# Optimization experiments

Hardware: AMD Instinct MI355X
Metric: run time of the kernel (lower is better)

The kernel has to match this reference:

```python
import jax, jax.numpy as jnp
import numpy as np

B, F, H, W, C = 1, 16, 32, 32, 128


def setup_inputs() -> dict:
    key = jax.random.key(0)
    ks = jax.random.split(key, 6)
    w = lambda k: jax.random.normal(k, (C, C), jnp.float32) * 0.02
    return {
        "x": jax.random.normal(ks[0], (B, F, H, W, C), jnp.float32),
        "gamma": jnp.ones((C,), jnp.float32),
        "wq": w(ks[1]), "bq": jnp.zeros((C,), jnp.float32),
        "wk": w(ks[2]), "bk": jnp.zeros((C,), jnp.float32),
        "wv": w(ks[3]), "bv": jnp.zeros((C,), jnp.float32),
        "wo": w(ks[4]), "bo": jnp.zeros((C,), jnp.float32),
    }


def reference(x, gamma, wq, bq, wk, bk, wv, bv, wo, bo):
    b, f, h, w_, c = x.shape
    s, n_hw = f * h * w_, h * w_
    identity = x

    # RMSNorm variant: L2-normalize over channels, rescale by sqrt(C) * gamma
    xn = x / (jnp.linalg.norm(x, axis=-1, keepdims=True) + 1e-8)
    xn = xn * (c ** 0.5) * gamma

    # 1x1x1 convs == pointwise linear projections; flatten to tokens [b, s, c]
    xn = xn.reshape(b, s, c)
    q = xn @ wq + bq
    k = xn @ wk + bk
    v = xn @ wv + bv

    # frame-causal block mask: query at frame i attends to all keys in frames <= i
    frame = jnp.arange(s) // n_hw                      # [s]
    allowed = frame[:, None] >= frame[None, :]          # [s, s] bool

    scale = 1.0 / jnp.sqrt(c)
    scores = jnp.einsum('bqc,bkc->bqk', q, k) * scale   # [b, s, s]
    scores = jnp.where(allowed, scores, -jnp.inf)
    attn = jax.nn.softmax(scores, axis=-1)
    out = jnp.einsum('bqk,bkc->bqc', attn, v)           # [b, s, c]

    out = out @ wo + bo
    return out.reshape(b, f, h, w_, c) + identity
```

## Files before the change

### kernel.cpp

```cpp
#include <hip/hip_runtime.h>
#include <hip/hip_bf16.h>

typedef __bf16 bf16x8 __attribute__((ext_vector_type(8)));
typedef float f32x4 __attribute__((ext_vector_type(4)));
typedef float f32x16 __attribute__((ext_vector_type(16)));
typedef unsigned short u16;
typedef unsigned int u32;
typedef u16 ushort8 __attribute__((ext_vector_type(8)));
typedef u32 u32x4 __attribute__((ext_vector_type(4)));

#define S_TOK 16384
#define C_DIM 128
#define L2E 1.4426950408889634f
#define QK_SCALE 0.08838834764831845f
#define SQRTC 11.313708498984761f

#define NBLK 512
#define TPB 34

#define WT_OFF   0u
#define BIAS_OFF 131072u
#define XN_OFF   147456u
#define O_OFF    XN_OFF
#define Q_OFF    (XN_OFF + 4194304u)
#define K_OFF    (Q_OFF + 4194304u)
#define VF_OFF   (K_OFF + 4194304u)
#define PART_OFF (VF_OFF + 4194304u)
#define ML_OFF   (PART_OFF + 20971520u)

#define ZERO16 ((f32x16){0.f,0.f,0.f,0.f,0.f,0.f,0.f,0.f,0.f,0.f,0.f,0.f,0.f,0.f,0.f,0.f})

__device__ __forceinline__ int in_is_bf16(const void* gamma) {
  return ((const u16*)gamma)[0] == 0x3F80;
}
__device__ __forceinline__ float ldf(const void* p, int i, int bf) {
  if (bf) { u32 b = ((const u16*)p)[i]; return __uint_as_float(b << 16); }
  return ((const float*)p)[i];
}
__device__ __forceinline__ float b2f(u16 b) { return __uint_as_float((u32)b << 16); }
__device__ __forceinline__ u16 f2b(float f) {
  return __builtin_bit_cast(u16, (__bf16)f);
}
__device__ __forceinline__ void gld16(const void* g, void* l) {
  __builtin_amdgcn_global_load_lds((const __attribute__((address_space(1))) u32*)g,
                                   (__attribute__((address_space(3))) u32*)l, 16, 0, 0);
}
__device__ __forceinline__ int qb_of(int t) {
  int F = 0;
  while (64 * (F + 1) * (F + 2) <= t) F++;
  int span = 16 * (F + 1);
  return 8 * F + (t - 64 * F * (F + 1)) / span;
}
__device__ __forceinline__ int start_of(int qq) {
  int Fq = qq >> 3, iq = qq & 7;
  return 16 * (Fq + 1) * (4 * Fq + iq);
}

__global__ void __launch_bounds__(256) prep_norm_kernel(const void* x, const void* gamma,
    const void* wq, const void* bq, const void* wk, const void* bk,
    const void* wv, const void* bv, const void* wo, const void* bo, char* ws) {
  int bf = in_is_bf16(gamma);
  if (blockIdx.x >= 2048) {
    int bb = blockIdx.x - 2048;
    if (bb < 256) {
      int gid = bb * 256 + threadIdx.x;
      int m = gid >> 14; int rem = gid & 16383;
      int k = rem >> 7; int n = rem & 127;
      const void* W = (m == 0) ? wq : (m == 1) ? wk : (m == 2) ? wv : wo;
      float v = ldf(W, rem, bf);
      if (m == 0) v *= QK_SCALE;
      *(u16*)(ws + WT_OFF + (u32)m * 32768u + (u32)n * 256u + (((u32)k * 2u) ^ (u32)((n & 7) << 4))) = f2b(v);
    } else {
      int idx = (bb - 256) * 256 + threadIdx.x;
      if (idx < 512) {
        int m = idx >> 7; int c = idx & 127;
        const void* B = (m == 0) ? bq : (m == 1) ? bk : (m == 2) ? bv : bo;
        float v = ldf(B, c, bf);
        if (m == 0) v *= QK_SCALE;
        ((float*)(ws + BIAS_OFF))[idx] = v;
      }
    }
    return;
  }
  int t = blockIdx.x * 256 + threadIdx.x;
  int tok = t >> 5; int sub = t & 31;
  int base = tok * 128 + sub * 4;
  float f[4];
  if (bf) {
    ushort4 v = ((const ushort4*)x)[base >> 2];
    f[0] = __uint_as_float((u32)v.x << 16); f[1] = __uint_as_float((u32)v.y << 16);
    f[2] = __uint_as_float((u32)v.z << 16); f[3] = __uint_as_float((u32)v.w << 16);
  } else {
    float4 v = ((const float4*)x)[base >> 2];
    f[0] = v.x; f[1] = v.y; f[2] = v.z; f[3] = v.w;
  }
  float ss = f[0]*f[0] + f[1]*f[1] + f[2]*f[2] + f[3]*f[3];
  #pragma unroll
  for (int m = 1; m < 32; m <<= 1) ss += __shfl_xor(ss, m);
  float fac = SQRTC / (sqrtf(ss) + 1e-8f);
  u16 o[4];
  #pragma unroll
  for (int j = 0; j < 4; j++) { float g = ldf(gamma, sub * 4 + j, bf); o[j] = f2b(f[j] * fac * g); }
  *(ushort4*)(ws + XN_OFF + (u32)tok * 256u + (((u32)sub * 8u) ^ (u32)((tok & 7) << 4))) =
      make_ushort4(o[0], o[1], o[2], o[3]);
}

__global__ void __launch_bounds__(256) qkv_kernel(char* ws) {
  __shared__ char lds[65536];
  int tid = threadIdx.x; int wid = tid >> 6; int lane = tid & 63;
  int blk = blockIdx.x & 127;
  int m = blockIdx.x >> 7;
  #pragma unroll
  for (int i = 0; i < 8; i++) {
    u32 seg = (u32)(i * 4 + wid) * 1024u;
    gld16(ws + XN_OFF + (u32)blk * 32768u + seg + (u32)lane * 16u, lds + seg);
    gld16(ws + WT_OFF + (u32)m * 32768u + seg + (u32)lane * 16u, lds + 32768 + seg);
  }
  __syncthreads();
  const float* bias = (const float*)(ws + BIAS_OFF);
  int rb = wid * 32;
  f32x4 acc[2][8];
  #pragma unroll
  for (int a = 0; a < 2; a++)
    #pragma unroll
    for (int b = 0; b < 8; b++) acc[a][b] = (f32x4){0.f, 0.f, 0.f, 0.f};
  #pragma unroll
  for (int kt = 0; kt < 4; kt++) {
    bf16x8 afr[2];
    #pragma unroll
    for (int mt = 0; mt < 2; mt++) {
      int row = rb + mt * 16 + (lane & 15);
      afr[mt] = *(const bf16x8*)(lds + row * 256 + ((kt * 64 + ((lane >> 4) * 16)) ^ ((row & 7) << 4)));
    }
    #pragma unroll
    for (int nt = 0; nt < 8; nt++) {
      int nr = nt * 16 + (lane & 15);
      bf16x8 bfr = *(const bf16x8*)(lds + 32768 + nr * 256 + ((kt * 64 + ((lane >> 4) * 16)) ^ ((nr & 7) << 4)));
      #pragma unroll
      for (int mt = 0; mt < 2; mt++)
        acc[mt][nt] = __builtin_amdgcn_mfma_f32_16x16x32_bf16(afr[mt], bfr, acc[mt][nt], 0, 0, 0);
    }
  }
  #pragma unroll
  for (int mt = 0; mt < 2; mt++)
    #pragma unroll
    for (int nt = 0; nt < 8; nt++) {
      int tok0 = blk * 128 + rb + mt * 16 + (lane >> 4) * 4;
      int c = (lane & 15) + nt * 16;
      float bv_ = bias[m * 128 + c];
      if (m == 0) {
        #pragma unroll
        for (int r = 0; r < 4; r++)
          *(u16*)(ws + Q_OFF + ((u32)(tok0 + r) * 128u + (u32)c) * 2u) = f2b(acc[mt][nt][r] + bv_);
      } else if (m == 1) {
        char* bp = ws + K_OFF + (u32)(tok0 >> 6) * 16384u
                 + (u32)((((tok0 >> 5) & 1) << 3) + (c >> 4)) * 1024u
                 + (u32)((tok0 & 31) + 32 * ((c >> 3) & 1)) * 16u + (u32)(c & 7) * 2u;
        #pragma unroll
        for (int r = 0; r < 4; r++)
          *(u16*)(bp + r * 16) = f2b(acc[mt][nt][r] + bv_);
      } else {
        u16 pk[4];
        #pragma unroll
        for (int r = 0; r < 4; r++) pk[r] = f2b(acc[mt][nt][r] + bv_);
        *(ushort4*)(ws + VF_OFF + (u32)(tok0 >> 6) * 16384u
                    + (u32)(((c >> 5) << 2) + ((tok0 >> 4) & 3)) * 1024u
                    + (u32)((c & 31) + 32 * ((tok0 >> 3) & 1)) * 16u + (u32)(tok0 & 7) * 2u)
            = make_ushort4(pk[0], pk[1], pk[2], pk[3]);
      }
    }
}

__global__ void __launch_bounds__(256, 2) attn_part_kernel(char* ws) {
  __shared__ char lds[65536];
  int tid = threadIdx.x; int wid = tid >> 6; int lane = tid & 63;
  int q = lane & 31; int hi = lane >> 5;
  int b = blockIdx.x;
  int slot = b;
  for (int qq = 1; qq < 128; qq++) {
    int Sx = start_of(qq);
    if (Sx < TPB * b && (Sx % TPB) != 0) slot++;
  }
  ushort8 ones_u;
  #pragma unroll
  for (int e = 0; e < 8; e++) ones_u[e] = 0x3F80;
  bf16x8 ones = __builtin_bit_cast(bf16x8, ones_u);

  auto stageK = [&](int t, int buf) {
    #pragma unroll
    for (int i = 0; i < 4; i++) {
      u32 off = (u32)(i * 4096) + (u32)tid * 16u;
      gld16(ws + K_OFF + (u32)t * 16384u + off, lds + buf * 16384 + off);
    }
  };
  auto stageV = [&](int t, int buf) {
    #pragma unroll
    for (int i = 0; i < 4; i++) {
      u32 off = (u32)(i * 4096) + (u32)tid * 16u;
      gld16(ws + VF_OFF + (u32)t * 16384u + off, lds + 32768 + buf * 16384 + off);
    }
  };

  int t0 = TPB * b, remaining = TPB;
  while (remaining > 0) {
    int F = 0;
    while (64 * (F + 1) * (F + 2) <= t0) F++;
    int fb = 64 * F * (F + 1); int span = 16 * (F + 1);
    int i = (t0 - fb) / span; int l = t0 - fb - i * span;
    int qb = 8 * F + i;
    int nt = min(remaining, span - l);

    bf16x8 aq[8];
    {
      const char* qp = ws + Q_OFF + (u32)(qb * 128 + wid * 32 + q) * 256u + (u32)(hi * 16);
      #pragma unroll
      for (int kt = 0; kt < 8; kt++) aq[kt] = *(const bf16x8*)(qp + kt * 32);
    }
    f32x16 acc0 = ZERO16, acc1 = ZERO16, acc2 = ZERO16, acc3 = ZERO16, accl = ZERO16;
    float m_run = -1e30f;
    float mL2 = m_run * L2E;

    __syncthreads();
    stageK(l, 0); stageV(l, 0);
    for (int it = 0; it < nt; it++) {
      int cur = it & 1;
      __syncthreads();
      if (it + 1 < nt) { stageK(l + it + 1, cur ^ 1); stageV(l + it + 1, cur ^ 1); }
      const char* kb_ = lds + cur * 16384;
      const char* vb_ = lds + 32768 + cur * 16384;
      f32x16 s0 = ZERO16, s1 = ZERO16;
      __builtin_amdgcn_s_setprio(1);
      #pragma unroll
      for (int kt = 0; kt < 8; kt++) {
        bf16x8 k0 = *(const bf16x8*)(kb_ + (0 * 8 + kt) * 1024 + (u32)lane * 16u);
        bf16x8 k1 = *(const bf16x8*)(kb_ + (1 * 8 + kt) * 1024 + (u32)lane * 16u);
        s0 = __builtin_amdgcn_mfma_f32_32x32x16_bf16(k0, aq[kt], s0, 0, 0, 0);
        s1 = __builtin_amdgcn_mfma_f32_32x32x16_bf16(k1, aq[kt], s1, 0, 0, 0);
      }
      __builtin_amdgcn_s_setprio(0);
      float tm = s0[0];
      #pragma unroll
      for (int r = 1; r < 16; r++) tm = fmaxf(tm, s0[r]);
      #pragma unroll
      for (int r = 0; r < 16; r++) tm = fmaxf(tm, s1[r]);
      tm = fmaxf(tm, __shfl_xor(tm, 32));
      if (__any(tm > m_run + 8.0f)) {
        float mnew = fmaxf(m_run, tm);
        float alpha = exp2f((m_run - mnew) * L2E);
        #pragma unroll
        for (int r = 0; r < 16; r++) {
          acc0[r] *= alpha; acc1[r] *= alpha; acc2[r] *= alpha; acc3[r] *= alpha; accl[r] *= alpha;
        }
        m_run = mnew; mL2 = m_run * L2E;
      }
      u32 W[16];
      #pragma unroll
      for (int t = 0; t < 8; t++) {
        float pa = exp2f(__builtin_fmaf(s0[2 * t], L2E, -mL2));
        float pb = exp2f(__builtin_fmaf(s0[2 * t + 1], L2E, -mL2));
        asm("v_cvt_pk_bf16_f32 %0, %1, %2" : "=v"(W[t]) : "v"(pa), "v"(pb));
      }
      #pragma unroll
      for (int t = 0; t < 8; t++) {
        float pa = exp2f(__builtin_fmaf(s1[2 * t], L2E, -mL2));
        float pb = exp2f(__builtin_fmaf(s1[2 * t + 1], L2E, -mL2));
        asm("v_cvt_pk_bf16_f32 %0, %1, %2" : "=v"(W[8 + t]) : "v"(pa), "v"(pb));
      }
      __builtin_amdgcn_s_setprio(1);
      #pragma unroll
      for (int kq = 0; kq < 4; kq++) {
        int base = (kq >> 1) * 8 + (kq & 1) * 4;
        u32 e0 = W[base + 0], e2 = W[base + 2];
        u32 e1 = W[base + 1], e3 = W[base + 3];
        asm("v_permlane32_swap_b32 %0, %1" : "+v"(e2), "+v"(e0));
        asm("v_permlane32_swap_b32 %0, %1" : "+v"(e3), "+v"(e1));
        u32x4 pw = (u32x4){e0, e1, e2, e3};
        bf16x8 pfr = __builtin_bit_cast(bf16x8, pw);
        accl = __builtin_amdgcn_mfma_f32_32x32x16_bf16(ones, pfr, accl, 0, 0, 0);
        bf16x8 v0 = *(const bf16x8*)(vb_ + (0 * 4 + kq) * 1024 + (u32)lane * 16u);
        bf16x8 v1 = *(const bf16x8*)(vb_ + (1 * 4 + kq) * 1024 + (u32)lane * 16u);
        bf16x8 v2 = *(const bf16x8*)(vb_ + (2 * 4 + kq) * 1024 + (u32)lane * 16u);
        bf16x8 v3 = *(const bf16x8*)(vb_ + (3 * 4 + kq) * 1024 + (u32)lane * 16u);
        acc0 = __builtin_amdgcn_mfma_f32_32x32x16_bf16(v0, pfr, acc0, 0, 0, 0);
        acc1 = __builtin_amdgcn_mfma_f32_32x32x16_bf16(v1, pfr, acc1, 0, 0, 0);
        acc2 = __builtin_amdgcn_mfma_f32_32x32x16_bf16(v2, pfr, acc2, 0, 0, 0);
        acc3 = __builtin_amdgcn_mfma_f32_32x32x16_bf16(v3, pfr, acc3, 0, 0, 0);
      }
      __builtin_amdgcn_s_setprio(0);
    }
    float l_run = accl[0];
    float rinv = 1.0f / l_run;
    int lrow = wid * 32 + q;
    char* pb2 = ws + PART_OFF + (u32)slot * 32768u + (u32)lrow * 256u;
    #pragma unroll
    for (int cb = 0; cb < 4; cb++) {
      const f32x16* A = (cb == 0) ? &acc0 : (cb == 1) ? &acc1 : (cb == 2) ? &acc2 : &acc3;
      #pragma unroll
      for (int t = 0; t < 8; t++) {
        float fa = (*A)[2 * t] * rinv, fb = (*A)[2 * t + 1] * rinv;
        u32 w;
        asm("v_cvt_pk_bf16_f32 %0, %1, %2" : "=v"(w) : "v"(fa), "v"(fb));
        int ch = cb * 32 + 8 * (t >> 1) + 2 * (t & 1) + 4 * hi;
        *(u32*)(pb2 + ch * 2) = w;
      }
    }
    if (hi == 0) ((float2*)(ws + ML_OFF))[slot * 128 + lrow] = make_float2(m_run, l_run);
    t0 += nt; remaining -= nt; slot++;
  }
}

__global__ void __launch_bounds__(256) combine_kernel(char* ws) {
  int qb = blockIdx.x >> 2;
  int seg = blockIdx.x & 3;
  int Sq = start_of(qb);
  int Eq = Sq + 16 * ((qb >> 3) + 1);
  int c_lo = Sq / TPB, c_hi = (Eq - 1) / TPB;
  int bse0 = c_lo;
  for (int qq = 1; qq < 128; qq++) {
    int Sx = start_of(qq);
    if (Sx < TPB * c_lo && (Sx % TPB) != 0) bse0++;
  }
  int tid = threadIdx.x;
  int row = seg * 32 + (tid >> 3);
  int oct = tid & 7;
  const float2* ml = (const float2*)(ws + ML_OFF);
  float M = -1e30f;
  {
    int bse = bse0;
    for (int c = c_lo; c <= c_hi; c++) {
      int qbf = qb_of(TPB * c);
      int qbl = qb_of(TPB * c + TPB - 1);
      int slot = bse + (qb - qbf);
      M = fmaxf(M, ml[slot * 128 + row].x);
      bse += qbl - qbf + 1;
    }
  }
  float a[16];
  #pragma unroll
  for (int k = 0; k < 16; k++) a[k] = 0.f;
  float D = 0.f;
  {
    int bse = bse0;
    for (int c = c_lo; c <= c_hi; c++) {
      int qbf = qb_of(TPB * c);
      int qbl = qb_of(TPB * c + TPB - 1);
      int slot = bse + (qb - qbf);
      bse += qbl - qbf + 1;
      float2 m_l = ml[slot * 128 + row];
      float w = exp2f((m_l.x - M) * L2E) * m_l.y;
      D += w;
      const u16* o = (const u16*)(ws + PART_OFF + (u32)slot * 32768u + (u32)row * 256u + (u32)oct * 32u);
      ushort8 v0 = *(const ushort8*)o;
      ushort8 v1 = *(const ushort8*)(o + 8);
      #pragma unroll
      for (int e = 0; e < 8; e++) { a[e] += w * b2f(v0[e]); a[8 + e] += w * b2f(v1[e]); }
    }
  }
  float Dinv = 1.0f / D;
  int grow = qb * 128 + row;
  ushort8 w0, w1;
  #pragma unroll
  for (int e = 0; e < 8; e++) { w0[e] = f2b(a[e] * Dinv); w1[e] = f2b(a[8 + e] * Dinv); }
  u32 rbase = (u32)grow * 256u;
  u32 swz = (u32)((row & 7) << 4);
  *(ushort8*)(ws + O_OFF + rbase + (((u32)oct * 32u) ^ swz)) = w0;
  *(ushort8*)(ws + O_OFF + rbase + (((u32)oct * 32u + 16u) ^ swz)) = w1;
}

__global__ void __launch_bounds__(256) out_kernel(const void* x, const void* gamma, char* ws, void* out) {
  __shared__ char lds[65536];
  int bf = in_is_bf16(gamma);
  int tid = threadIdx.x; int wid = tid >> 6; int lane = tid & 63;
  int blk = blockIdx.x;
  #pragma unroll
  for (int i = 0; i < 8; i++) {
    u32 seg = (u32)(i * 4 + wid) * 1024u;
    gld16(ws + O_OFF + (u32)blk * 32768u + seg + (u32)lane * 16u, lds + seg);
    gld16(ws + WT_OFF + 3u * 32768u + seg + (u32)lane * 16u, lds + 32768 + seg);
  }
  __syncthreads();
  f32x4 acc[2][8];
  #pragma unroll
  for (int a = 0; a < 2; a++)
    #pragma unroll
    for (int b = 0; b < 8; b++) acc[a][b] = (f32x4){0.f, 0.f, 0.f, 0.f};
  int rb = wid * 32;
  #pragma unroll
  for (int kt = 0; kt < 4; kt++) {
    bf16x8 afr[2];
    #pragma unroll
    for (int mt = 0; mt < 2; mt++) {
      int row = rb + mt * 16 + (lane & 15);
      afr[mt] = *(const bf16x8*)(lds + row * 256 + ((kt * 64 + ((lane >> 4) * 16)) ^ ((row & 7) << 4)));
    }
    #pragma unroll
    for (int nt = 0; nt < 8; nt++) {
      int nr = nt * 16 + (lane & 15);
      bf16x8 bfr = *(const bf16x8*)(lds + 32768 + nr * 256 + ((kt * 64 + ((lane >> 4) * 16)) ^ ((nr & 7) << 4)));
      #pragma unroll
      for (int mt = 0; mt < 2; mt++)
        acc[mt][nt] = __builtin_amdgcn_mfma_f32_16x16x32_bf16(afr[mt], bfr, acc[mt][nt], 0, 0, 0);
    }
  }
  const float* bias = (const float*)(ws + BIAS_OFF) + 3 * 128;
  #pragma unroll
  for (int mt = 0; mt < 2; mt++)
    #pragma unroll
    for (int nt = 0; nt < 8; nt++) {
      int c = (lane & 15) + nt * 16;
      float bv_ = bias[c];
      #pragma unroll
      for (int r = 0; r < 4; r++) {
        int tok = blk * 128 + rb + mt * 16 + (lane >> 4) * 4 + r;
        float v = acc[mt][nt][r] + bv_ + ldf(x, tok * 128 + c, bf);
        if (bf) ((u16*)out)[tok * 128 + c] = f2b(v);
        else    ((float*)out)[tok * 128 + c] = v;
      }
    }
}

extern "C" void kernel_launch(void* const* d_in, const int* in_sizes, int n_in,
                              void* d_out, int out_size, void* d_ws, size_t ws_size,
                              hipStream_t stream) {
  (void)in_sizes; (void)n_in; (void)out_size; (void)ws_size;
  const void* x     = d_in[0];
  const void* gamma = d_in[1];
  const void* wq = d_in[2]; const void* bq = d_in[3];
  const void* wk = d_in[4]; const void* bk = d_in[5];
  const void* wv = d_in[6]; const void* bv = d_in[7];
  const void* wo = d_in[8]; const void* bo = d_in[9];
  char* ws = (char*)d_ws;
  hipLaunchKernelGGL(prep_norm_kernel, dim3(2306), dim3(256), 0, stream,
                     x, gamma, wq, bq, wk, bk, wv, bv, wo, bo, ws);
  hipLaunchKernelGGL(qkv_kernel, dim3(384), dim3(256), 0, stream, ws);
  hipLaunchKernelGGL(attn_part_kernel, dim3(NBLK), dim3(256), 0, stream, ws);
  hipLaunchKernelGGL(combine_kernel, dim3(512), dim3(256), 0, stream, ws);
  hipLaunchKernelGGL(out_kernel, dim3(128), dim3(256), 0, stream, x, gamma, ws, d_out);
}
```

Before: 175.7 us.

## Process 256-query super-blocks per attention block to reuse K/V tiles

Each attention work item now covers 256 query rows (two 32-row sub-tiles per wave) instead of 128, so every K/V tile staged into LDS feeds twice as many MFMAs and the total K/V global traffic is halved. Tokens per block drop from 34 to 17 to keep the work split balanced, and the partial buffer and combine indexing are resized for the new super-block scheme. The row sum is now accumulated with VALU adds and shuffles instead of an extra MFMA against a ones vector, and exp2 uses raw v_exp_f32. The cost is much higher register pressure from doubled accumulators and Q fragments, which may reduce occupancy or cause spills.

```diff
diff --git a/kernel.cpp b/kernel.cpp
--- a/kernel.cpp
+++ b/kernel.cpp
@@ -16,7 +16,7 @@
 #define SQRTC 11.313708498984761f
 
 #define NBLK 512
-#define TPB 34
+#define TPB 17
 
 #define WT_OFF   0u
 #define BIAS_OFF 131072u
@@ -26,7 +26,7 @@
 #define K_OFF    (Q_OFF + 4194304u)
 #define VF_OFF   (K_OFF + 4194304u)
 #define PART_OFF (VF_OFF + 4194304u)
-#define ML_OFF   (PART_OFF + 20971520u)
+#define ML_OFF   (PART_OFF + 37748736u)
 
 #define ZERO16 ((f32x16){0.f,0.f,0.f,0.f,0.f,0.f,0.f,0.f,0.f,0.f,0.f,0.f,0.f,0.f,0.f,0.f})
 
@@ -41,19 +41,22 @@
 __device__ __forceinline__ u16 f2b(float f) {
   return __builtin_bit_cast(u16, (__bf16)f);
 }
+__device__ __forceinline__ float fexp2(float x) {
+  float y; asm("v_exp_f32 %0, %1" : "=v"(y) : "v"(x)); return y;
+}
 __device__ __forceinline__ void gld16(const void* g, void* l) {
   __builtin_amdgcn_global_load_lds((const __attribute__((address_space(1))) u32*)g,
                                    (__attribute__((address_space(3))) u32*)l, 16, 0, 0);
 }
 __device__ __forceinline__ int qb_of(int t) {
   int F = 0;
-  while (64 * (F + 1) * (F + 2) <= t) F++;
+  while (32 * (F + 1) * (F + 2) <= t) F++;
   int span = 16 * (F + 1);
-  return 8 * F + (t - 64 * F * (F + 1)) / span;
-}
-__device__ __forceinline__ int start_of(int qq) {
-  int Fq = qq >> 3, iq = qq & 7;
-  return 16 * (Fq + 1) * (4 * Fq + iq);
+  return 4 * F + (t - 32 * F * (F + 1)) / span;
+}
+__device__ __forceinline__ int start_of(int ss) {
+  int Fq = ss >> 2, iq = ss & 3;
+  return 16 * (Fq + 1) * (2 * Fq + iq);
 }
 
 __global__ void __launch_bounds__(256) prep_norm_kernel(const void* x, const void* gamma,
@@ -177,14 +180,10 @@
   int q = lane & 31; int hi = lane >> 5;
   int b = blockIdx.x;
   int slot = b;
-  for (int qq = 1; qq < 128; qq++) {
-    int Sx = start_of(qq);
+  for (int ss = 1; ss < 64; ss++) {
+    int Sx = start_of(ss);
     if (Sx < TPB * b && (Sx % TPB) != 0) slot++;
   }
-  ushort8 ones_u;
-  #pragma unroll
-  for (int e = 0; e < 8; e++) ones_u[e] = 0x3F80;
-  bf16x8 ones = __builtin_bit_cast(bf16x8, ones_u);
 
   auto stageK = [&](int t, int buf) {
     #pragma unroll
@@ -204,21 +203,25 @@
   int t0 = TPB * b, remaining = TPB;
   while (remaining > 0) {
     int F = 0;
-    while (64 * (F + 1) * (F + 2) <= t0) F++;
-    int fb = 64 * F * (F + 1); int span = 16 * (F + 1);
+    while (32 * (F + 1) * (F + 2) <= t0) F++;
+    int fb = 32 * F * (F + 1); int span = 16 * (F + 1);
     int i = (t0 - fb) / span; int l = t0 - fb - i * span;
-    int qb = 8 * F + i;
+    int sb = 4 * F + i;
     int nt = min(remaining, span - l);
 
-    bf16x8 aq[8];
+    bf16x8 aq0[8], aq1[8];
     {
-      const char* qp = ws + Q_OFF + (u32)(qb * 128 + wid * 32 + q) * 256u + (u32)(hi * 16);
-      #pragma unroll
-      for (int kt = 0; kt < 8; kt++) aq[kt] = *(const bf16x8*)(qp + kt * 32);
-    }
-    f32x16 acc0 = ZERO16, acc1 = ZERO16, acc2 = ZERO16, acc3 = ZERO16, accl = ZERO16;
-    float m_run = -1e30f;
-    float mL2 = m_run * L2E;
+      const char* qp = ws + Q_OFF + (u32)(sb * 256 + wid * 64 + q) * 256u + (u32)(hi * 16);
+      #pragma unroll
+      for (int kt = 0; kt < 8; kt++) {
+        aq0[kt] = *(const bf16x8*)(qp + kt * 32);
+        aq1[kt] = *(const bf16x8*)(qp + 8192 + kt * 32);
+      }
+    }
+    f32x16 a00 = ZERO16, a01 = ZERO16, a02 = ZERO16, a03 = ZERO16;
+    f32x16 a10 = ZERO16, a11 = ZERO16, a12 = ZERO16, a13 = ZERO16;
+    float m0 = -1e30f, m1 = -1e30f, lr0 = 0.f, lr1 = 0.f;
+    float mL0 = m0 * L2E, mL1 = m1 * L2E;
 
     __syncthreads();
     stageK(l, 0); stageV(l, 0);
@@ -228,96 +231,164 @@
       if (it + 1 < nt) { stageK(l + it + 1, cur ^ 1); stageV(l + it + 1, cur ^ 1); }
       const char* kb_ = lds + cur * 16384;
       const char* vb_ = lds + 32768 + cur * 16384;
-      f32x16 s0 = ZERO16, s1 = ZERO16;
-      __builtin_amdgcn_s_setprio(1);
-      #pragma unroll
-      for (int kt = 0; kt < 8; kt++) {
-        bf16x8 k0 = *(const bf16x8*)(kb_ + (0 * 8 + kt) * 1024 + (u32)lane * 16u);
-        bf16x8 k1 = *(const bf16x8*)(kb_ + (1 * 8 + kt) * 1024 + (u32)lane * 16u);
-        s0 = __builtin_amdgcn_mfma_f32_32x32x16_bf16(k0, aq[kt], s0, 0, 0, 0);
-        s1 = __builtin_amdgcn_mfma_f32_32x32x16_bf16(k1, aq[kt], s1, 0, 0, 0);
-      }
-      __builtin_amdgcn_s_setprio(0);
-      float tm = s0[0];
-      #pragma unroll
-      for (int r = 1; r < 16; r++) tm = fmaxf(tm, s0[r]);
-      #pragma unroll
-      for (int r = 0; r < 16; r++) tm = fmaxf(tm, s1[r]);
-      tm = fmaxf(tm, __shfl_xor(tm, 32));
-      if (__any(tm > m_run + 8.0f)) {
-        float mnew = fmaxf(m_run, tm);
-        float alpha = exp2f((m_run - mnew) * L2E);
-        #pragma unroll
-        for (int r = 0; r < 16; r++) {
-          acc0[r] *= alpha; acc1[r] *= alpha; acc2[r] *= alpha; acc3[r] *= alpha; accl[r] *= alpha;
-        }
-        m_run = mnew; mL2 = m_run * L2E;
-      }
-      u32 W[16];
-      #pragma unroll
-      for (int t = 0; t < 8; t++) {
-        float pa = exp2f(__builtin_fmaf(s0[2 * t], L2E, -mL2));
-        float pb = exp2f(__builtin_fmaf(s0[2 * t + 1], L2E, -mL2));
-        asm("v_cvt_pk_bf16_f32 %0, %1, %2" : "=v"(W[t]) : "v"(pa), "v"(pb));
-      }
-      #pragma unroll
-      for (int t = 0; t < 8; t++) {
-        float pa = exp2f(__builtin_fmaf(s1[2 * t], L2E, -mL2));
-        float pb = exp2f(__builtin_fmaf(s1[2 * t + 1], L2E, -mL2));
-        asm("v_cvt_pk_bf16_f32 %0, %1, %2" : "=v"(W[8 + t]) : "v"(pa), "v"(pb));
+      u32 W0[16], W1[16];
+      {
+        f32x16 s0 = ZERO16, s1 = ZERO16;
+        __builtin_amdgcn_s_setprio(1);
+        #pragma unroll
+        for (int kt = 0; kt < 8; kt++) {
+          bf16x8 k0 = *(const bf16x8*)(kb_ + kt * 1024 + (u32)lane * 16u);
+          bf16x8 k1 = *(const bf16x8*)(kb_ + (8 + kt) * 1024 + (u32)lane * 16u);
+          s0 = __builtin_amdgcn_mfma_f32_32x32x16_bf16(k0, aq0[kt], s0, 0, 0, 0);
+          s1 = __builtin_amdgcn_mfma_f32_32x32x16_bf16(k1, aq0[kt], s1, 0, 0, 0);
+        }
+        __builtin_amdgcn_s_setprio(0);
+        float tm = s0[0];
+        #pragma unroll
+        for (int r = 1; r < 16; r++) tm = fmaxf(tm, s0[r]);
+        #pragma unroll
+        for (int r = 0; r < 16; r++) tm = fmaxf(tm, s1[r]);
+        tm = fmaxf(tm, __shfl_xor(tm, 32));
+        if (__any(tm > m0 + 8.0f)) {
+          float mnew = fmaxf(m0, tm);
+          float alpha = fexp2((m0 - mnew) * L2E);
+          #pragma unroll
+          for (int r = 0; r < 16; r++) { a00[r] *= alpha; a01[r] *= alpha; a02[r] *= alpha; a03[r] *= alpha; }
+          lr0 *= alpha; m0 = mnew; mL0 = m0 * L2E;
+        }
+        float ps = 0.f;
+        #pragma unroll
+        for (int t = 0; t < 8; t++) {
+          float pa = fexp2(__builtin_fmaf(s0[2 * t], L2E, -mL0));
+          float pb = fexp2(__builtin_fmaf(s0[2 * t + 1], L2E, -mL0));
+          ps += pa + pb;
+          asm("v_cvt_pk_bf16_f32 %0, %1, %2" : "=v"(W0[t]) : "v"(pa), "v"(pb));
+        }
+        #pragma unroll
+        for (int t = 0; t < 8; t++) {
+          float pa = fexp2(__builtin_fmaf(s1[2 * t], L2E, -mL0));
+          float pb = fexp2(__builtin_fmaf(s1[2 * t + 1], L2E, -mL0));
+          ps += pa + pb;
+          asm("v_cvt_pk_bf16_f32 %0, %1, %2" : "=v"(W0[8 + t]) : "v"(pa), "v"(pb));
+        }
+        ps += __shfl_xor(ps, 32);
+        lr0 += ps;
+      }
+      asm volatile("" ::: "memory");
+      {
+        f32x16 s0 = ZERO16, s1 = ZERO16;
+        __builtin_amdgcn_s_setprio(1);
+        #pragma unroll
+        for (int kt = 0; kt < 8; kt++) {
+          bf16x8 k0 = *(const bf16x8*)(kb_ + kt * 1024 + (u32)lane * 16u);
+          bf16x8 k1 = *(const bf16x8*)(kb_ + (8 + kt) * 1024 + (u32)lane * 16u);
+          s0 = __builtin_amdgcn_mfma_f32_32x32x16_bf16(k0, aq1[kt], s0, 0, 0, 0);
+          s1 = __builtin_amdgcn_mfma_f32_32x32x16_bf16(k1, aq1[kt], s1, 0, 0, 0);
+        }
+        __builtin_amdgcn_s_setprio(0);
+        float tm = s0[0];
+        #pragma unroll
+        for (int r = 1; r < 16; r++) tm = fmaxf(tm, s0[r]);
+        #pragma unroll
+        for (int r = 0; r < 16; r++) tm = fmaxf(tm, s1[r]);
+        tm = fmaxf(tm, __shfl_xor(tm, 32));
+        if (__any(tm > m1 + 8.0f)) {
+          float mnew = fmaxf(m1, tm);
+          float alpha = fexp2((m1 - mnew) * L2E);
+          #pragma unroll
+          for (int r = 0; r < 16; r++) { a10[r] *= alpha; a11[r] *= alpha; a12[r] *= alpha; a13[r] *= alpha; }
+          lr1 *= alpha; m1 = mnew; mL1 = m1 * L2E;
+        }
+        float ps = 0.f;
+        #pragma unroll
+        for (int t = 0; t < 8; t++) {
+          float pa = fexp2(__builtin_fmaf(s0[2 * t], L2E, -mL1));
+          float pb = fexp2(__builtin_fmaf(s0[2 * t + 1], L2E, -mL1));
+          ps += pa + pb;
+          asm("v_cvt_pk_bf16_f32 %0, %1, %2" : "=v"(W1[t]) : "v"(pa), "v"(pb));
+        }
+        #pragma unroll
+        for (int t = 0; t < 8; t++) {
+          float pa = fexp2(__builtin_fmaf(s1[2 * t], L2E, -mL1));
+          float pb = fexp2(__builtin_fmaf(s1[2 * t + 1], L2E, -mL1));
+          ps += pa + pb;
+          asm("v_cvt_pk_bf16_f32 %0, %1, %2" : "=v"(W1[8 + t]) : "v"(pa), "v"(pb));
+        }
+        ps += __shfl_xor(ps, 32);
+        lr1 += ps;
       }
       __builtin_amdgcn_s_setprio(1);
       #pragma unroll
       for (int kq = 0; kq < 4; kq++) {
         int base = (kq >> 1) * 8 + (kq & 1) * 4;
-        u32 e0 = W[base + 0], e2 = W[base + 2];
-        u32 e1 = W[base + 1], e3 = W[base + 3];
+        u32 e0 = W0[base + 0], e2 = W0[base + 2];
+        u32 e1 = W0[base + 1], e3 = W0[base + 3];
         asm("v_permlane32_swap_b32 %0, %1" : "+v"(e2), "+v"(e0));
         asm("v_permlane32_swap_b32 %0, %1" : "+v"(e3), "+v"(e1));
-        u32x4 pw = (u32x4){e0, e1, e2, e3};
-        bf16x8 pfr = __builtin_bit_cast(bf16x8, pw);
-        accl = __builtin_amdgcn_mfma_f32_32x32x16_bf16(ones, pfr, accl, 0, 0, 0);
+        u32x4 pw0 = (u32x4){e0, e1, e2, e3};
+        bf16x8 pfr0 = __builtin_bit_cast(bf16x8, pw0);
+        u32 f0 = W1[base + 0], f2 = W1[base + 2];
+        u32 f1 = W1[base + 1], f3 = W1[base + 3];
+        asm("v_permlane32_swap_b32 %0, %1" : "+v"(f2), "+v"(f0));
+        asm("v_permlane32_swap_b32 %0, %1" : "+v"(f3), "+v"(f1));
+        u32x4 pw1 = (u32x4){f0, f1, f2, f3};
+        bf16x8 pfr1 = __builtin_bit_cast(bf16x8, pw1);
         bf16x8 v0 = *(const bf16x8*)(vb_ + (0 * 4 + kq) * 1024 + (u32)lane * 16u);
         bf16x8 v1 = *(const bf16x8*)(vb_ + (1 * 4 + kq) * 1024 + (u32)lane * 16u);
         bf16x8 v2 = *(const bf16x8*)(vb_ + (2 * 4 + kq) * 1024 + (u32)lane * 16u);
         bf16x8 v3 = *(const bf16x8*)(vb_ + (3 * 4 + kq) * 1024 + (u32)lane * 16u);
-        acc0 = __builtin_amdgcn_mfma_f32_32x32x16_bf16(v0, pfr, acc0, 0, 0, 0);
-        acc1 = __builtin_amdgcn_mfma_f32_32x32x16_bf16(v1, pfr, acc1, 0, 0, 0);
-        acc2 = __builtin_amdgcn_mfma_f32_32x32x16_bf16(v2, pfr, acc2, 0, 0, 0);
-        acc3 = __builtin_amdgcn_mfma_f32_32x32x16_bf16(v3, pfr, acc3, 0, 0, 0);
+        a00 = __builtin_amdgcn_mfma_f32_32x32x16_bf16(v0, pfr0, a00, 0, 0, 0);
+        a10 = __builtin_amdgcn_mfma_f32_32x32x16_bf16(v0, pfr1, a10, 0, 0, 0);
+        a01 = __builtin_amdgcn_mfma_f32_32x32x16_bf16(v1, pfr0, a01, 0, 0, 0);
+        a11 = __builtin_amdgcn_mfma_f32_32x32x16_bf16(v1, pfr1, a11, 0, 0, 0);
+        a02 = __builtin_amdgcn_mfma_f32_32x32x16_bf16(v2, pfr0, a02, 0, 0, 0);
+        a12 = __builtin_amdgcn_mfma_f32_32x32x16_bf16(v2, pfr1, a12, 0, 0, 0);
+        a03 = __builtin_amdgcn_mfma_f32_32x32x16_bf16(v3, pfr0, a03, 0, 0, 0);
+        a13 = __builtin_amdgcn_mfma_f32_32x32x16_bf16(v3, pfr1, a13, 0, 0, 0);
       }
       __builtin_amdgcn_s_setprio(0);
     }
-    float l_run = accl[0];
-    float rinv = 1.0f / l_run;
-    int lrow = wid * 32 + q;
-    char* pb2 = ws + PART_OFF + (u32)slot * 32768u + (u32)lrow * 256u;
-    #pragma unroll
-    for (int cb = 0; cb < 4; cb++) {
-      const f32x16* A = (cb == 0) ? &acc0 : (cb == 1) ? &acc1 : (cb == 2) ? &acc2 : &acc3;
-      #pragma unroll
-      for (int t = 0; t < 8; t++) {
-        float fa = (*A)[2 * t] * rinv, fb = (*A)[2 * t + 1] * rinv;
-        u32 w;
-        asm("v_cvt_pk_bf16_f32 %0, %1, %2" : "=v"(w) : "v"(fa), "v"(fb));
-        int ch = cb * 32 + 8 * (t >> 1) + 2 * (t & 1) + 4 * hi;
-        *(u32*)(pb2 + ch * 2) = w;
-      }
-    }
-    if (hi == 0) ((float2*)(ws + ML_OFF))[slot * 128 + lrow] = make_float2(m_run, l_run);
+    {
+      float ri0 = 1.0f / lr0, ri1 = 1.0f / lr1;
+      int lrow0 = wid * 64 + q;
+      char* pb0 = ws + PART_OFF + (u32)slot * 65536u + (u32)lrow0 * 256u;
+      char* pb1 = pb0 + 32 * 256;
+      #pragma unroll
+      for (int cb = 0; cb < 4; cb++) {
+        const f32x16* A0 = (cb == 0) ? &a00 : (cb == 1) ? &a01 : (cb == 2) ? &a02 : &a03;
+        const f32x16* A1 = (cb == 0) ? &a10 : (cb == 1) ? &a11 : (cb == 2) ? &a12 : &a13;
+        #pragma unroll
+        for (int t = 0; t < 8; t++) {
+          int ch = cb * 32 + 8 * (t >> 1) + 2 * (t & 1) + 4 * hi;
+          float fa = (*A0)[2 * t] * ri0, fb = (*A0)[2 * t + 1] * ri0;
+          u32 w;
+          asm("v_cvt_pk_bf16_f32 %0, %1, %2" : "=v"(w) : "v"(fa), "v"(fb));
+          *(u32*)(pb0 + ch * 2) = w;
+          float ga = (*A1)[2 * t] * ri1, gb = (*A1)[2 * t + 1] * ri1;
+          u32 w2;
+          asm("v_cvt_pk_bf16_f32 %0, %1, %2" : "=v"(w2) : "v"(ga), "v"(gb));
+          *(u32*)(pb1 + ch * 2) = w2;
+        }
+      }
+      if (hi == 0) {
+        ((float2*)(ws + ML_OFF))[slot * 256 + lrow0] = make_float2(m0, lr0);
+        ((float2*)(ws + ML_OFF))[slot * 256 + lrow0 + 32] = make_float2(m1, lr1);
+      }
+    }
     t0 += nt; remaining -= nt; slot++;
   }
 }
 
 __global__ void __launch_bounds__(256) combine_kernel(char* ws) {
-  int qb = blockIdx.x >> 2;
-  int seg = blockIdx.x & 3;
-  int Sq = start_of(qb);
-  int Eq = Sq + 16 * ((qb >> 3) + 1);
+  int sb = blockIdx.x >> 3;
+  int seg = blockIdx.x & 7;
+  int F = sb >> 2;
+  int Sq = start_of(sb);
+  int Eq = Sq + 16 * (F + 1);
   int c_lo = Sq / TPB, c_hi = (Eq - 1) / TPB;
   int bse0 = c_lo;
-  for (int qq = 1; qq < 128; qq++) {
-    int Sx = start_of(qq);
+  for (int ss = 1; ss < 64; ss++) {
+    int Sx = start_of(ss);
     if (Sx < TPB * c_lo && (Sx % TPB) != 0) bse0++;
   }
   int tid = threadIdx.x;
@@ -328,11 +399,11 @@
   {
     int bse = bse0;
     for (int c = c_lo; c <= c_hi; c++) {
-      int qbf = qb_of(TPB * c);
-      int qbl = qb_of(TPB * c + TPB - 1);
-      int slot = bse + (qb - qbf);
-      M = fmaxf(M, ml[slot * 128 + row].x);
-      bse += qbl - qbf + 1;
+      int sbf = qb_of(TPB * c);
+      int sbl = qb_of(TPB * c + TPB - 1);
+      int slot = bse + (sb - sbf);
+      M = fmaxf(M, ml[slot * 256 + row].x);
+      bse += sbl - sbf + 1;
     }
   }
   float a[16];
@@ -342,14 +413,14 @@
   {
     int bse = bse0;
     for (int c = c_lo; c <= c_hi; c++) {
-      int qbf = qb_of(TPB * c);
-      int qbl = qb_of(TPB * c + TPB - 1);
-      int slot = bse + (qb - qbf);
-      bse += qbl - qbf + 1;
-      float2 m_l = ml[slot * 128 + row];
+      int sbf = qb_of(TPB * c);
+      int sbl = qb_of(TPB * c + TPB - 1);
+      int slot = bse + (sb - sbf);
+      bse += sbl - sbf + 1;
+      float2 m_l = ml[slot * 256 + row];
       float w = exp2f((m_l.x - M) * L2E) * m_l.y;
       D += w;
-      const u16* o = (const u16*)(ws + PART_OFF + (u32)slot * 32768u + (u32)row * 256u + (u32)oct * 32u);
+      const u16* o = (const u16*)(ws + PART_OFF + (u32)slot * 65536u + (u32)row * 256u + (u32)oct * 32u);
       ushort8 v0 = *(const ushort8*)o;
       ushort8 v1 = *(const ushort8*)(o + 8);
       #pragma unroll
@@ -357,7 +428,7 @@
     }
   }
   float Dinv = 1.0f / D;
-  int grow = qb * 128 + row;
+  int grow = sb * 256 + row;
   ushort8 w0, w1;
   #pragma unroll
   for (int e = 0; e < 8; e++) { w0[e] = f2b(a[e] * Dinv); w1[e] = f2b(a[8 + e] * Dinv); }
```

Measured after the change: 217.6 us. 23.9% more time.
